# Kernel tuning notes

Measured on AMD Instinct MI355X. Metric: run time of the kernel, lower is better.

The kernel has to match this reference:

```python
import jax, jax.numpy as jnp
import numpy as np

TOPK = 5
LAMBDA_ALIGN_K = 16.0
MOM = 0.9          # EMA momentum
DEFAULT_SCORE = 0.5  # EMA bank default (bank starts empty)
EPS = 1e-8
NEG = 1.0e9


def pairwise_cosine(X):
    # torch F.normalize: X / max(||X||, eps)
    n = jnp.linalg.norm(X, axis=-1, keepdims=True)
    Xn = X / jnp.maximum(n, EPS)
    sim = Xn @ Xn.T
    return jnp.clip(sim, -1.0 + EPS, 1.0 - EPS)


def knn_mask(sim, allowed_base, topk=TOPK):
    B = sim.shape[0]
    eye = jnp.eye(B, dtype=sim.dtype)
    allowed = allowed_base * (1.0 - eye)
    masked = sim - NEG * eye
    masked = jnp.where(allowed < 0.5, -NEG, masked)
    masked = jnp.where(masked < 0.0, -NEG, masked)
    cand = (masked > 0).sum(axis=1)
    k = min(topk, max(B - 1, 1))
    keep_row = (cand >= topk).astype(sim.dtype)
    keep = keep_row[:, None] * keep_row[None, :]
    idx = jax.lax.top_k(masked, k)[1]                       # [B, k]
    M = jnp.zeros_like(sim).at[jnp.arange(B)[:, None], idx].set(1.0)
    M = jnp.maximum(M, M.T)
    return M * allowed * keep


def build_intra(sim, same, topk=TOPK):
    M = knn_mask(sim, same, topk)
    A = jnp.maximum(sim * M, 0.0) * same
    return A, M


def pga_loss(feats_sub, labels_sub):
    # feats_sub: [L, b, d]
    L = feats_sub.shape[0]
    same = (labels_sub[:, None] == labels_sub[None, :]).astype(jnp.float32)
    sims = jax.vmap(pairwise_cosine)(feats_sub)             # [L, b, b]
    A, M = jax.vmap(lambda s: build_intra(s, same))(sims)   # [L, b, b] each

    # EMA degree-based scores (no-grad in original; bank starts empty so
    # fetch-after-update == mom*default + (1-mom)*score_cur)
    S_intra = jnp.maximum(sims * same, 0.0)
    deg = jnp.maximum((S_intra > 0).sum(axis=2).astype(jnp.float32), 1.0)
    score_cur = jax.nn.sigmoid(S_intra.sum(axis=2) / deg)   # [L, b]
    ema = jax.lax.stop_gradient(MOM * DEFAULT_SCORE + (1.0 - MOM) * score_cur)

    # layer-pair masked MSE alignment, target detached
    A_deep = A[1:]
    A_tgt = jax.lax.stop_gradient(A[:-1])
    M_eff = jnp.maximum(M[:-1], M[1:])                      # [L-1, b, b]
    W = ema[:-1, :, None] * ema[:-1, None, :]               # [L-1, b, b]
    diff2 = (A_deep - A_tgt) ** 2 * W
    num = (diff2 * M_eff).sum(axis=(1, 2))
    den = jnp.maximum((M_eff * W).sum(axis=(1, 2)), EPS)
    terms = jnp.where(M_eff.sum(axis=(1, 2)) > 0, num / den, 0.0)
    raw = terms.sum() / max(L - 1, 1)
    return LAMBDA_ALIGN_K * raw


def setup_inputs() -> dict:
    key = jax.random.key(0)
    k1, k2 = jax.random.split(key)
    feats_final = jax.random.normal(k1, (8, 2048, 512), dtype=jnp.float32)
    labels = jax.random.randint(k2, (2048,), 0, 128).astype(jnp.int64)
    sample_ids = jnp.arange(2048, dtype=jnp.int64)
    return {"feats_final": feats_final, "labels": labels, "sample_ids": sample_ids}


def reference(feats_final, labels, sample_ids):
    # candidate subset from last layer (no-grad in original)
    X_last = feats_final[-1]
    S_last = pairwise_cosine(X_last)
    same_full = (labels[:, None] == labels[None, :]).astype(jnp.float32)
    _, M_last = build_intra(S_last, same_full)
    cand_mask = (M_last > 0).sum(axis=1) > 0
    idx_sub = jnp.nonzero(cand_mask)[0]  # eager (concrete) subselection
    feats_sub = feats_final[:, idx_sub]  # [L, b, d]
    labels_sub = labels[idx_sub]
    return pga_loss(feats_sub, labels_sub)
```

## Files before the change

### kernel.cpp

```cpp
#include <hip/hip_runtime.h>
#include <cmath>

#define NB   2048
#define ND   512
#define NL   8
#define NLAB 128
#define MAXM 64
#define TOPK_ 5
#define NTH  256
#define MAXSLOT 9
#define GSTRIDE (MAXM*MAXM)

__global__ __launch_bounds__(NTH) void k_bucket(
    const int* __restrict__ labels, int* __restrict__ members,
    int* __restrict__ cnt)
{
    __shared__ int cnts[NTH];
    int c = blockIdx.x, tid = threadIdx.x;
    int my[8]; int n = 0;
    int base_i = tid * 8;
    for (int t = 0; t < 8; ++t) {
        int i = base_i + t;
        if (labels[i] == c) my[n++] = i;
    }
    cnts[tid] = n;
    __syncthreads();
    for (int off = 1; off < NTH; off <<= 1) {
        int v = (tid >= off) ? cnts[tid - off] : 0;
        __syncthreads();
        cnts[tid] += v;
        __syncthreads();
    }
    int excl = cnts[tid] - n;
    if (tid == 0) cnt[c] = cnts[NTH - 1];
    for (int t = 0; t < n; ++t) {
        int slot = excl + t;
        if (slot < MAXM) members[c * MAXM + slot] = my[t];
    }
}

__global__ __launch_bounds__(NTH) void k_gram(
    const float* __restrict__ feats, const int* __restrict__ members,
    const int* __restrict__ cnt, float* __restrict__ G)
{
    __shared__ float Xt[MAXM][132];
    __shared__ int g_s[MAXM];
    int c = blockIdx.x, l = blockIdx.y, tid = threadIdx.x;
    int m = cnt[c]; if (m > MAXM) m = MAXM;
    if (m == 0) return;
    if (tid < m) g_s[tid] = members[c * MAXM + tid];
    __syncthreads();
    const float* X = feats + (size_t)l * NB * ND;

    const int P = m * (m + 1) / 2;
    float acc0[MAXSLOT], acc1[MAXSLOT];
    short is_[MAXSLOT], js_[MAXSLOT];
    int ns = 0;
    for (int p = tid; p < P; p += NTH) {
        int i = (int)((sqrtf(8.0f * (float)p + 1.0f) - 1.0f) * 0.5f);
        while (((i + 1) * (i + 2)) / 2 <= p) ++i;
        while ((i * (i + 1)) / 2 > p) --i;
        is_[ns] = (short)i;
        js_[ns] = (short)(p - (i * (i + 1)) / 2);
        acc0[ns] = 0.0f; acc1[ns] = 0.0f;
        ++ns;
    }
    for (int kc = 0; kc < ND; kc += 128) {
        if (kc) __syncthreads();
        for (int idx = tid; idx < (m << 5); idx += NTH) {
            int i = idx >> 5, k4 = idx & 31;
            float4 v = *(const float4*)(X + ((size_t)g_s[i] << 9) + kc + (k4 << 2));
            *(float4*)&Xt[i][k4 << 2] = v;
        }
        __syncthreads();
        for (int s = 0; s < ns; ++s) {
            int i = is_[s], j = js_[s];
            float a0 = acc0[s], a1 = acc1[s];
            #pragma unroll
            for (int k4 = 0; k4 < 32; ++k4) {
                float4 a = *(const float4*)&Xt[i][k4 << 2];
                float4 b = *(const float4*)&Xt[j][k4 << 2];
                a0 = fmaf(a.x, b.x, a0); a1 = fmaf(a.y, b.y, a1);
                a0 = fmaf(a.z, b.z, a0); a1 = fmaf(a.w, b.w, a1);
            }
            acc0[s] = a0; acc1[s] = a1;
        }
    }
    float* Gc = G + ((size_t)l * NLAB + c) * GSTRIDE;
    for (int s = 0; s < ns; ++s) {
        int i = is_[s], j = js_[s];
        float v = acc0[s] + acc1[s];
        Gc[i * MAXM + j] = v;
        Gc[j * MAXM + i] = v;
    }
}

__global__ __launch_bounds__(NTH) void k_phase1(
    const float* __restrict__ G, const int* __restrict__ cnt,
    unsigned long long* __restrict__ insub)
{
    __shared__ float Gs[64][65];
    __shared__ float rinv[64];
    __shared__ unsigned long long tops_s[64];
    __shared__ unsigned char keep_s[64];
    int c = blockIdx.x, tid = threadIdx.x;
    int m = cnt[c]; if (m > MAXM) m = MAXM;
    if (m == 0) { if (tid == 0) insub[c] = 0ull; return; }
    const float* Gc = G + ((size_t)7 * NLAB + c) * GSTRIDE;
    if (tid < m) rinv[tid] = 1.0f / fmaxf(sqrtf(Gc[tid * MAXM + tid]), 1e-8f);
    __syncthreads();
    for (int idx = tid; idx < (m << 6); idx += NTH) {
        int i = idx >> 6, j = idx & 63;
        if (j < m) {
            float v = Gc[idx] * rinv[i] * rinv[j];
            Gs[i][j] = fminf(fmaxf(v, -1.0f), 1.0f);
        }
    }
    __syncthreads();

    unsigned long long tops = 0ull; bool keep = false;
    if (tid < m) {
        int cand = 0;
        for (int j = 0; j < m; ++j)
            if (j != tid && Gs[tid][j] > 0.0f) ++cand;
        keep = (cand >= TOPK_);
        if (keep) {
            for (int r = 0; r < TOPK_; ++r) {
                float bv = 0.0f; int bj = -1;
                for (int j = 0; j < m; ++j) {
                    if (j == tid || ((tops >> j) & 1ull)) continue;
                    float v = Gs[tid][j];
                    if (v > 0.0f && v > bv) { bv = v; bj = j; }
                }
                if (bj >= 0) tops |= (1ull << bj);
            }
        }
        keep_s[tid] = keep ? 1 : 0; tops_s[tid] = tops;
    }
    __syncthreads();
    unsigned long long Mrow = 0ull;
    if (tid < m && keep) {
        for (int j = 0; j < m; ++j) {
            if (j == tid || !keep_s[j]) continue;
            if (((tops >> j) & 1ull) || ((tops_s[j] >> tid) & 1ull)) Mrow |= (1ull << j);
        }
    }
    if (tid < 64) {
        unsigned long long b = __ballot(Mrow != 0ull);
        if (tid == 0) insub[c] = b;
    }
}

__global__ __launch_bounds__(NTH) void k_decide(
    const float* __restrict__ G, const int* __restrict__ cnt,
    const unsigned long long* __restrict__ insub,
    unsigned long long* __restrict__ Mbits, float* __restrict__ ema)
{
    __shared__ float Gs[64][65];
    __shared__ float rinv[64];
    __shared__ unsigned long long tops_s[64];
    __shared__ unsigned char keep_s[64];
    int c = blockIdx.x, l = blockIdx.y, tid = threadIdx.x;
    int m = cnt[c]; if (m > MAXM) m = MAXM;
    if (m == 0) return;
    unsigned long long sub = insub[c];
    const float* Gc = G + ((size_t)l * NLAB + c) * GSTRIDE;
    if (tid < m) rinv[tid] = 1.0f / fmaxf(sqrtf(Gc[tid * MAXM + tid]), 1e-8f);
    __syncthreads();
    for (int idx = tid; idx < (m << 6); idx += NTH) {
        int i = idx >> 6, j = idx & 63;
        if (j < m) {
            float v = Gc[idx] * rinv[i] * rinv[j];
            Gs[i][j] = fminf(fmaxf(v, -1.0f), 1.0f);
        }
    }
    __syncthreads();

    unsigned long long tops = 0ull; bool keep = false; bool act = false;
    if (tid < m) {
        act = (sub >> tid) & 1ull;
        int cand = 0;
        if (act) {
            for (int j = 0; j < m; ++j)
                if (j != tid && ((sub >> j) & 1ull) && Gs[tid][j] > 0.0f) ++cand;
        }
        keep = act && (cand >= TOPK_);
        if (keep) {
            for (int r = 0; r < TOPK_; ++r) {
                float bv = 0.0f; int bj = -1;
                for (int j = 0; j < m; ++j) {
                    if (j == tid || !((sub >> j) & 1ull) || ((tops >> j) & 1ull)) continue;
                    float v = Gs[tid][j];
                    if (v > 0.0f && v > bv) { bv = v; bj = j; }
                }
                if (bj >= 0) tops |= (1ull << bj);
            }
        }
        keep_s[tid] = keep ? 1 : 0; tops_s[tid] = tops;
    }
    __syncthreads();
    if (tid < m) {
        unsigned long long Mrow = 0ull;
        if (keep) {
            for (int j = 0; j < m; ++j) {
                if (j == tid || !keep_s[j]) continue;
                if (((tops >> j) & 1ull) || ((tops_s[j] >> tid) & 1ull)) Mrow |= (1ull << j);
            }
        }
        Mbits[((size_t)l * NLAB + c) * MAXM + tid] = Mrow;
        float emaval = 0.0f;
        if (act) {
            float rs = 0.0f; int dg = 0;
            for (int j = 0; j < m; ++j) {
                if ((sub >> j) & 1ull) {
                    float v = Gs[tid][j];
                    if (v > 0.0f) { rs += v; ++dg; }
                }
            }
            float deg = (float)(dg > 0 ? dg : 1);
            float score = 1.0f / (1.0f + expf(-rs / deg));
            emaval = 0.45f + 0.1f * score;
        }
        ema[((size_t)l * NLAB + c) * MAXM + tid] = emaval;
    }
}

__global__ __launch_bounds__(NTH) void k_pairs(
    const float* __restrict__ G, const int* __restrict__ cnt,
    const unsigned long long* __restrict__ Mbits, const float* __restrict__ ema,
    float* __restrict__ partial)
{
    __shared__ float r0[64], r1[64];
    __shared__ unsigned long long M0s[64], M1s[64];
    __shared__ float es[64];
    __shared__ float red[12];
    int c = blockIdx.x, p = blockIdx.y, tid = threadIdx.x;
    int m = cnt[c]; if (m > MAXM) m = MAXM;
    const float* G0 = G + ((size_t)p       * NLAB + c) * GSTRIDE;
    const float* G1 = G + ((size_t)(p + 1) * NLAB + c) * GSTRIDE;
    if (tid < m) {
        M0s[tid] = Mbits[((size_t)p * NLAB + c) * MAXM + tid];
        M1s[tid] = Mbits[((size_t)(p + 1) * NLAB + c) * MAXM + tid];
        es[tid]  = ema[((size_t)p * NLAB + c) * MAXM + tid];
        r0[tid]  = 1.0f / fmaxf(sqrtf(G0[tid * MAXM + tid]), 1e-8f);
        r1[tid]  = 1.0f / fmaxf(sqrtf(G1[tid * MAXM + tid]), 1e-8f);
    }
    __syncthreads();
    float fn = 0.0f, fd = 0.0f, fc = 0.0f;
    for (int idx = tid; idx < (m << 6); idx += NTH) {
        int i = idx >> 6, j = idx & 63;
        if (j >= m) continue;
        bool b0 = (M0s[i] >> j) & 1ull;
        bool b1 = (M1s[i] >> j) & 1ull;
        if (b0 | b1) {
            float v0 = b0 ? fminf(fmaxf(G0[idx] * r0[i] * r0[j], -1.0f), 1.0f) : 0.0f;
            float v1 = b1 ? fminf(fmaxf(G1[idx] * r1[i] * r1[j], -1.0f), 1.0f) : 0.0f;
            float w = es[i] * es[j];
            float d = v1 - v0;
            fn = fmaf(d * d, w, fn);
            fd += w;
            fc += 1.0f;
        }
    }
    for (int off = 32; off > 0; off >>= 1) {
        fn += __shfl_down(fn, off);
        fd += __shfl_down(fd, off);
        fc += __shfl_down(fc, off);
    }
    int w = tid >> 6;
    if ((tid & 63) == 0) { red[w * 3] = fn; red[w * 3 + 1] = fd; red[w * 3 + 2] = fc; }
    __syncthreads();
    if (tid == 0) {
        float* dst = partial + ((size_t)p * NLAB + c) * 4;
        dst[0] = red[0] + red[3] + red[6] + red[9];
        dst[1] = red[1] + red[4] + red[7] + red[10];
        dst[2] = red[2] + red[5] + red[8] + red[11];
    }
}

__global__ void k_final(const float* __restrict__ partial, float* __restrict__ out)
{
    int tid = threadIdx.x;
    float total = 0.0f;
    for (int p = 0; p < NL - 1; ++p) {
        float n = 0.0f, d = 0.0f, cc = 0.0f;
        for (int c = tid; c < NLAB; c += 64) {
            const float* src = partial + ((size_t)p * NLAB + c) * 4;
            n += src[0]; d += src[1]; cc += src[2];
        }
        for (int off = 32; off > 0; off >>= 1) {
            n += __shfl_down(n, off);
            d += __shfl_down(d, off);
            cc += __shfl_down(cc, off);
        }
        if (tid == 0 && cc > 0.0f) total += n / fmaxf(d, 1e-8f);
    }
    if (tid == 0) out[0] = 16.0f * total / 7.0f;
}

extern "C" void kernel_launch(void* const* d_in, const int* in_sizes, int n_in,
                              void* d_out, int out_size, void* d_ws, size_t ws_size,
                              hipStream_t stream) {
    const float* feats  = (const float*)d_in[0];
    const int*   labels = (const int*)d_in[1];
    char* w = (char*)d_ws;
    int* members              = (int*)(w);
    int* cnt                  = (int*)(w + 32768);
    unsigned long long* insub = (unsigned long long*)(w + 33280);
    unsigned long long* Mbits = (unsigned long long*)(w + 34304);
    float* ema                = (float*)(w + 558592);
    float* G                  = (float*)(w + 821248);
    float* partial            = (float*)(w + 821248 + (size_t)NL * NLAB * GSTRIDE * 4);
    float* out                = (float*)d_out;

    k_bucket<<<NLAB, NTH, 0, stream>>>(labels, members, cnt);
    k_gram  <<<dim3(NLAB, NL), NTH, 0, stream>>>(feats, members, cnt, G);
    k_phase1<<<NLAB, NTH, 0, stream>>>(G, cnt, insub);
    k_decide<<<dim3(NLAB, NL), NTH, 0, stream>>>(G, cnt, insub, Mbits, ema);
    k_pairs <<<dim3(NLAB, NL - 1), NTH, 0, stream>>>(G, cnt, Mbits, ema, partial);
    k_final <<<1, 64, 0, stream>>>(partial, out);
}
```

Measured before the change: 147.0 us.

## Fuse six kernels into two: bucket into gram, post-gram stages into one per-label kernel

Label bucketing is folded into the Gram kernel, so each block scans labels itself instead of reading a separate members array. Phase1, per-layer decide, pair alignment and the final reduction are merged into one kernel with a block per label, which keeps masks and EMA values in shared memory. A ticket atomic lets the last finishing block do the global reduction. This removes four launches and the global round trips for intermediates, but the per-label work now runs on only 128 blocks in sequence over layers instead of 1024 parallel blocks.

```diff
diff --git a/kernel.cpp b/kernel.cpp
--- a/kernel.cpp
+++ b/kernel.cpp
@@ -11,14 +11,17 @@
 #define MAXSLOT 9
 #define GSTRIDE (MAXM*MAXM)
 
-__global__ __launch_bounds__(NTH) void k_bucket(
-    const int* __restrict__ labels, int* __restrict__ members,
-    int* __restrict__ cnt)
+__global__ __launch_bounds__(NTH) void k_gram(
+    const float* __restrict__ feats, const int* __restrict__ labels,
+    float* __restrict__ G, unsigned* __restrict__ ticket)
 {
     __shared__ int cnts[NTH];
-    int c = blockIdx.x, tid = threadIdx.x;
-    int my[8]; int n = 0;
-    int base_i = tid * 8;
+    __shared__ int g_s[MAXM];
+    __shared__ float Xt[MAXM][132];
+    int c = blockIdx.x, l = blockIdx.y, tid = threadIdx.x;
+    if (c == 0 && l == 0 && tid == 0) *ticket = 0u;
+
+    int my[8]; int n = 0; int base_i = tid * 8;
     for (int t = 0; t < 8; ++t) {
         int i = base_i + t;
         if (labels[i] == c) my[n++] = i;
@@ -32,26 +35,15 @@
         __syncthreads();
     }
     int excl = cnts[tid] - n;
-    if (tid == 0) cnt[c] = cnts[NTH - 1];
+    int m = cnts[NTH - 1]; if (m > MAXM) m = MAXM;
     for (int t = 0; t < n; ++t) {
         int slot = excl + t;
-        if (slot < MAXM) members[c * MAXM + slot] = my[t];
-    }
-}
-
-__global__ __launch_bounds__(NTH) void k_gram(
-    const float* __restrict__ feats, const int* __restrict__ members,
-    const int* __restrict__ cnt, float* __restrict__ G)
-{
-    __shared__ float Xt[MAXM][132];
-    __shared__ int g_s[MAXM];
-    int c = blockIdx.x, l = blockIdx.y, tid = threadIdx.x;
-    int m = cnt[c]; if (m > MAXM) m = MAXM;
+        if (slot < MAXM) g_s[slot] = my[t];
+    }
+    __syncthreads();
     if (m == 0) return;
-    if (tid < m) g_s[tid] = members[c * MAXM + tid];
-    __syncthreads();
+
     const float* X = feats + (size_t)l * NB * ND;
-
     const int P = m * (m + 1) / 2;
     float acc0[MAXSLOT], acc1[MAXSLOT];
     short is_[MAXSLOT], js_[MAXSLOT];
@@ -95,207 +87,210 @@
     }
 }
 
-__global__ __launch_bounds__(NTH) void k_phase1(
-    const float* __restrict__ G, const int* __restrict__ cnt,
-    unsigned long long* __restrict__ insub)
+__global__ __launch_bounds__(NTH) void k_rest(
+    const float* __restrict__ G, const int* __restrict__ labels,
+    float* __restrict__ partial,
+    unsigned* __restrict__ ticket, float* __restrict__ out)
 {
     __shared__ float Gs[64][65];
-    __shared__ float rinv[64];
+    __shared__ float rinv8[NL][64];
+    __shared__ unsigned long long Mb[NL][64];
+    __shared__ float es8[NL][64];
     __shared__ unsigned long long tops_s[64];
     __shared__ unsigned char keep_s[64];
+    __shared__ int cnts[NTH];
+    __shared__ unsigned long long insub_sh;
+    __shared__ float red[12];
+    __shared__ unsigned done_s;
     int c = blockIdx.x, tid = threadIdx.x;
-    int m = cnt[c]; if (m > MAXM) m = MAXM;
-    if (m == 0) { if (tid == 0) insub[c] = 0ull; return; }
-    const float* Gc = G + ((size_t)7 * NLAB + c) * GSTRIDE;
-    if (tid < m) rinv[tid] = 1.0f / fmaxf(sqrtf(Gc[tid * MAXM + tid]), 1e-8f);
-    __syncthreads();
-    for (int idx = tid; idx < (m << 6); idx += NTH) {
-        int i = idx >> 6, j = idx & 63;
-        if (j < m) {
-            float v = Gc[idx] * rinv[i] * rinv[j];
-            Gs[i][j] = fminf(fmaxf(v, -1.0f), 1.0f);
-        }
-    }
-    __syncthreads();
-
-    unsigned long long tops = 0ull; bool keep = false;
-    if (tid < m) {
-        int cand = 0;
-        for (int j = 0; j < m; ++j)
-            if (j != tid && Gs[tid][j] > 0.0f) ++cand;
-        keep = (cand >= TOPK_);
-        if (keep) {
-            for (int r = 0; r < TOPK_; ++r) {
-                float bv = 0.0f; int bj = -1;
+
+    int n = 0; int base_i = tid * 8;
+    for (int t = 0; t < 8; ++t) if (labels[base_i + t] == c) ++n;
+    cnts[tid] = n;
+    __syncthreads();
+    for (int off = NTH / 2; off > 0; off >>= 1) {
+        if (tid < off) cnts[tid] += cnts[tid + off];
+        __syncthreads();
+    }
+    int m = cnts[0]; if (m > MAXM) m = MAXM;
+
+    if (m > 0) {
+        const float* Gc7 = G + ((size_t)7 * NLAB + c) * GSTRIDE;
+        if (tid < m) rinv8[7][tid] = 1.0f / fmaxf(sqrtf(Gc7[tid * MAXM + tid]), 1e-8f);
+        __syncthreads();
+        for (int idx = tid; idx < (m << 6); idx += NTH) {
+            int i = idx >> 6, j = idx & 63;
+            if (j < m) {
+                float v = Gc7[idx] * rinv8[7][i] * rinv8[7][j];
+                Gs[i][j] = fminf(fmaxf(v, -1.0f), 1.0f);
+            }
+        }
+        __syncthreads();
+        {
+            unsigned long long tops = 0ull; bool keep = false;
+            if (tid < m) {
+                int cand = 0;
+                for (int j = 0; j < m; ++j)
+                    if (j != tid && Gs[tid][j] > 0.0f) ++cand;
+                keep = (cand >= TOPK_);
+                if (keep) {
+                    for (int r = 0; r < TOPK_; ++r) {
+                        float bv = 0.0f; int bj = -1;
+                        for (int j = 0; j < m; ++j) {
+                            if (j == tid || ((tops >> j) & 1ull)) continue;
+                            float v = Gs[tid][j];
+                            if (v > 0.0f && v > bv) { bv = v; bj = j; }
+                        }
+                        if (bj >= 0) tops |= (1ull << bj);
+                    }
+                }
+                keep_s[tid] = keep ? 1 : 0; tops_s[tid] = tops;
+            }
+            __syncthreads();
+            unsigned long long Mrow = 0ull;
+            if (tid < m && keep) {
                 for (int j = 0; j < m; ++j) {
-                    if (j == tid || ((tops >> j) & 1ull)) continue;
-                    float v = Gs[tid][j];
-                    if (v > 0.0f && v > bv) { bv = v; bj = j; }
-                }
-                if (bj >= 0) tops |= (1ull << bj);
-            }
-        }
-        keep_s[tid] = keep ? 1 : 0; tops_s[tid] = tops;
-    }
-    __syncthreads();
-    unsigned long long Mrow = 0ull;
-    if (tid < m && keep) {
-        for (int j = 0; j < m; ++j) {
-            if (j == tid || !keep_s[j]) continue;
-            if (((tops >> j) & 1ull) || ((tops_s[j] >> tid) & 1ull)) Mrow |= (1ull << j);
-        }
-    }
-    if (tid < 64) {
-        unsigned long long b = __ballot(Mrow != 0ull);
-        if (tid == 0) insub[c] = b;
-    }
-}
-
-__global__ __launch_bounds__(NTH) void k_decide(
-    const float* __restrict__ G, const int* __restrict__ cnt,
-    const unsigned long long* __restrict__ insub,
-    unsigned long long* __restrict__ Mbits, float* __restrict__ ema)
-{
-    __shared__ float Gs[64][65];
-    __shared__ float rinv[64];
-    __shared__ unsigned long long tops_s[64];
-    __shared__ unsigned char keep_s[64];
-    int c = blockIdx.x, l = blockIdx.y, tid = threadIdx.x;
-    int m = cnt[c]; if (m > MAXM) m = MAXM;
-    if (m == 0) return;
-    unsigned long long sub = insub[c];
-    const float* Gc = G + ((size_t)l * NLAB + c) * GSTRIDE;
-    if (tid < m) rinv[tid] = 1.0f / fmaxf(sqrtf(Gc[tid * MAXM + tid]), 1e-8f);
-    __syncthreads();
-    for (int idx = tid; idx < (m << 6); idx += NTH) {
-        int i = idx >> 6, j = idx & 63;
-        if (j < m) {
-            float v = Gc[idx] * rinv[i] * rinv[j];
-            Gs[i][j] = fminf(fmaxf(v, -1.0f), 1.0f);
-        }
-    }
-    __syncthreads();
-
-    unsigned long long tops = 0ull; bool keep = false; bool act = false;
-    if (tid < m) {
-        act = (sub >> tid) & 1ull;
-        int cand = 0;
-        if (act) {
-            for (int j = 0; j < m; ++j)
-                if (j != tid && ((sub >> j) & 1ull) && Gs[tid][j] > 0.0f) ++cand;
-        }
-        keep = act && (cand >= TOPK_);
-        if (keep) {
-            for (int r = 0; r < TOPK_; ++r) {
-                float bv = 0.0f; int bj = -1;
-                for (int j = 0; j < m; ++j) {
-                    if (j == tid || !((sub >> j) & 1ull) || ((tops >> j) & 1ull)) continue;
-                    float v = Gs[tid][j];
-                    if (v > 0.0f && v > bv) { bv = v; bj = j; }
-                }
-                if (bj >= 0) tops |= (1ull << bj);
-            }
-        }
-        keep_s[tid] = keep ? 1 : 0; tops_s[tid] = tops;
-    }
-    __syncthreads();
-    if (tid < m) {
-        unsigned long long Mrow = 0ull;
-        if (keep) {
-            for (int j = 0; j < m; ++j) {
-                if (j == tid || !keep_s[j]) continue;
-                if (((tops >> j) & 1ull) || ((tops_s[j] >> tid) & 1ull)) Mrow |= (1ull << j);
-            }
-        }
-        Mbits[((size_t)l * NLAB + c) * MAXM + tid] = Mrow;
-        float emaval = 0.0f;
-        if (act) {
-            float rs = 0.0f; int dg = 0;
-            for (int j = 0; j < m; ++j) {
-                if ((sub >> j) & 1ull) {
-                    float v = Gs[tid][j];
-                    if (v > 0.0f) { rs += v; ++dg; }
-                }
-            }
-            float deg = (float)(dg > 0 ? dg : 1);
-            float score = 1.0f / (1.0f + expf(-rs / deg));
-            emaval = 0.45f + 0.1f * score;
-        }
-        ema[((size_t)l * NLAB + c) * MAXM + tid] = emaval;
-    }
-}
-
-__global__ __launch_bounds__(NTH) void k_pairs(
-    const float* __restrict__ G, const int* __restrict__ cnt,
-    const unsigned long long* __restrict__ Mbits, const float* __restrict__ ema,
-    float* __restrict__ partial)
-{
-    __shared__ float r0[64], r1[64];
-    __shared__ unsigned long long M0s[64], M1s[64];
-    __shared__ float es[64];
-    __shared__ float red[12];
-    int c = blockIdx.x, p = blockIdx.y, tid = threadIdx.x;
-    int m = cnt[c]; if (m > MAXM) m = MAXM;
-    const float* G0 = G + ((size_t)p       * NLAB + c) * GSTRIDE;
-    const float* G1 = G + ((size_t)(p + 1) * NLAB + c) * GSTRIDE;
-    if (tid < m) {
-        M0s[tid] = Mbits[((size_t)p * NLAB + c) * MAXM + tid];
-        M1s[tid] = Mbits[((size_t)(p + 1) * NLAB + c) * MAXM + tid];
-        es[tid]  = ema[((size_t)p * NLAB + c) * MAXM + tid];
-        r0[tid]  = 1.0f / fmaxf(sqrtf(G0[tid * MAXM + tid]), 1e-8f);
-        r1[tid]  = 1.0f / fmaxf(sqrtf(G1[tid * MAXM + tid]), 1e-8f);
-    }
-    __syncthreads();
-    float fn = 0.0f, fd = 0.0f, fc = 0.0f;
-    for (int idx = tid; idx < (m << 6); idx += NTH) {
-        int i = idx >> 6, j = idx & 63;
-        if (j >= m) continue;
-        bool b0 = (M0s[i] >> j) & 1ull;
-        bool b1 = (M1s[i] >> j) & 1ull;
-        if (b0 | b1) {
-            float v0 = b0 ? fminf(fmaxf(G0[idx] * r0[i] * r0[j], -1.0f), 1.0f) : 0.0f;
-            float v1 = b1 ? fminf(fmaxf(G1[idx] * r1[i] * r1[j], -1.0f), 1.0f) : 0.0f;
-            float w = es[i] * es[j];
-            float d = v1 - v0;
-            fn = fmaf(d * d, w, fn);
-            fd += w;
-            fc += 1.0f;
-        }
-    }
-    for (int off = 32; off > 0; off >>= 1) {
-        fn += __shfl_down(fn, off);
-        fd += __shfl_down(fd, off);
-        fc += __shfl_down(fc, off);
-    }
-    int w = tid >> 6;
-    if ((tid & 63) == 0) { red[w * 3] = fn; red[w * 3 + 1] = fd; red[w * 3 + 2] = fc; }
-    __syncthreads();
-    if (tid == 0) {
-        float* dst = partial + ((size_t)p * NLAB + c) * 4;
-        dst[0] = red[0] + red[3] + red[6] + red[9];
-        dst[1] = red[1] + red[4] + red[7] + red[10];
-        dst[2] = red[2] + red[5] + red[8] + red[11];
-    }
-}
-
-__global__ void k_final(const float* __restrict__ partial, float* __restrict__ out)
-{
-    int tid = threadIdx.x;
-    float total = 0.0f;
-    for (int p = 0; p < NL - 1; ++p) {
-        float n = 0.0f, d = 0.0f, cc = 0.0f;
-        for (int c = tid; c < NLAB; c += 64) {
-            const float* src = partial + ((size_t)p * NLAB + c) * 4;
-            n += src[0]; d += src[1]; cc += src[2];
-        }
-        for (int off = 32; off > 0; off >>= 1) {
-            n += __shfl_down(n, off);
-            d += __shfl_down(d, off);
-            cc += __shfl_down(cc, off);
-        }
-        if (tid == 0 && cc > 0.0f) total += n / fmaxf(d, 1e-8f);
-    }
-    if (tid == 0) out[0] = 16.0f * total / 7.0f;
+                    if (j == tid || !keep_s[j]) continue;
+                    if (((tops >> j) & 1ull) || ((tops_s[j] >> tid) & 1ull)) Mrow |= (1ull << j);
+                }
+            }
+            if (tid < 64) {
+                unsigned long long b = __ballot(Mrow != 0ull);
+                if (tid == 0) insub_sh = b;
+            }
+            __syncthreads();
+        }
+        unsigned long long sub = insub_sh;
+
+        for (int l = 0; l < NL; ++l) {
+            const float* Gc = G + ((size_t)l * NLAB + c) * GSTRIDE;
+            if (tid < m) rinv8[l][tid] = 1.0f / fmaxf(sqrtf(Gc[tid * MAXM + tid]), 1e-8f);
+            __syncthreads();
+            for (int idx = tid; idx < (m << 6); idx += NTH) {
+                int i = idx >> 6, j = idx & 63;
+                if (j < m) {
+                    float v = Gc[idx] * rinv8[l][i] * rinv8[l][j];
+                    Gs[i][j] = fminf(fmaxf(v, -1.0f), 1.0f);
+                }
+            }
+            __syncthreads();
+            unsigned long long tops = 0ull; bool keep = false; bool act = false;
+            if (tid < m) {
+                act = (sub >> tid) & 1ull;
+                int cand = 0;
+                if (act) {
+                    for (int j = 0; j < m; ++j)
+                        if (j != tid && ((sub >> j) & 1ull) && Gs[tid][j] > 0.0f) ++cand;
+                }
+                keep = act && (cand >= TOPK_);
+                if (keep) {
+                    for (int r = 0; r < TOPK_; ++r) {
+                        float bv = 0.0f; int bj = -1;
+                        for (int j = 0; j < m; ++j) {
+                            if (j == tid || !((sub >> j) & 1ull) || ((tops >> j) & 1ull)) continue;
+                            float v = Gs[tid][j];
+                            if (v > 0.0f && v > bv) { bv = v; bj = j; }
+                        }
+                        if (bj >= 0) tops |= (1ull << bj);
+                    }
+                }
+                keep_s[tid] = keep ? 1 : 0; tops_s[tid] = tops;
+            }
+            __syncthreads();
+            if (tid < m) {
+                unsigned long long Mrow = 0ull;
+                if (keep) {
+                    for (int j = 0; j < m; ++j) {
+                        if (j == tid || !keep_s[j]) continue;
+                        if (((tops >> j) & 1ull) || ((tops_s[j] >> tid) & 1ull)) Mrow |= (1ull << j);
+                    }
+                }
+                Mb[l][tid] = Mrow;
+                float emaval = 0.0f;
+                if (act) {
+                    float rs = 0.0f; int dg = 0;
+                    for (int j = 0; j < m; ++j) {
+                        if ((sub >> j) & 1ull) {
+                            float v = Gs[tid][j];
+                            if (v > 0.0f) { rs += v; ++dg; }
+                        }
+                    }
+                    float deg = (float)(dg > 0 ? dg : 1);
+                    float score = 1.0f / (1.0f + expf(-rs / deg));
+                    emaval = 0.45f + 0.1f * score;
+                }
+                es8[l][tid] = emaval;
+            }
+            __syncthreads();
+        }
+
+        for (int p = 0; p < NL - 1; ++p) {
+            const float* G0 = G + ((size_t)p       * NLAB + c) * GSTRIDE;
+            const float* G1 = G + ((size_t)(p + 1) * NLAB + c) * GSTRIDE;
+            float fn = 0.0f, fd = 0.0f, fc = 0.0f;
+            for (int idx = tid; idx < (m << 6); idx += NTH) {
+                int i = idx >> 6, j = idx & 63;
+                if (j >= m) continue;
+                bool b0 = (Mb[p][i] >> j) & 1ull;
+                bool b1 = (Mb[p + 1][i] >> j) & 1ull;
+                if (b0 | b1) {
+                    float v0 = b0 ? fminf(fmaxf(G0[idx] * rinv8[p][i] * rinv8[p][j], -1.0f), 1.0f) : 0.0f;
+                    float v1 = b1 ? fminf(fmaxf(G1[idx] * rinv8[p + 1][i] * rinv8[p + 1][j], -1.0f), 1.0f) : 0.0f;
+                    float w = es8[p][i] * es8[p][j];
+                    float d = v1 - v0;
+                    fn = fmaf(d * d, w, fn);
+                    fd += w;
+                    fc += 1.0f;
+                }
+            }
+            for (int off = 32; off > 0; off >>= 1) {
+                fn += __shfl_down(fn, off);
+                fd += __shfl_down(fd, off);
+                fc += __shfl_down(fc, off);
+            }
+            int w = tid >> 6;
+            if ((tid & 63) == 0) { red[w * 3] = fn; red[w * 3 + 1] = fd; red[w * 3 + 2] = fc; }
+            __syncthreads();
+            if (tid == 0) {
+                float* dst = partial + ((size_t)p * NLAB + c) * 4;
+                dst[0] = red[0] + red[3] + red[6] + red[9];
+                dst[1] = red[1] + red[4] + red[7] + red[10];
+                dst[2] = red[2] + red[5] + red[8] + red[11];
+            }
+            __syncthreads();
+        }
+    } else {
+        if (tid < NL - 1) {
+            float* dst = partial + ((size_t)tid * NLAB + c) * 4;
+            dst[0] = 0.0f; dst[1] = 0.0f; dst[2] = 0.0f;
+        }
+        __syncthreads();
+    }
+
+    __threadfence();
+    __syncthreads();
+    if (tid == 0) done_s = atomicAdd(ticket, 1u);
+    __syncthreads();
+    if (done_s == NLAB - 1) {
+        __threadfence();
+        if (tid < 64) {
+            float total = 0.0f;
+            for (int p = 0; p < NL - 1; ++p) {
+                float nn = 0.0f, dd = 0.0f, cc = 0.0f;
+                for (int cc_i = tid; cc_i < NLAB; cc_i += 64) {
+                    const float* src = partial + ((size_t)p * NLAB + cc_i) * 4;
+                    nn += src[0]; dd += src[1]; cc += src[2];
+                }
+                for (int off = 32; off > 0; off >>= 1) {
+                    nn += __shfl_down(nn, off);
+                    dd += __shfl_down(dd, off);
+                    cc += __shfl_down(cc, off);
+                }
+                if (tid == 0 && cc > 0.0f) total += nn / fmaxf(dd, 1e-8f);
+            }
+            if (tid == 0) out[0] = 16.0f * total / 7.0f;
+        }
+    }
 }
 
 extern "C" void kernel_launch(void* const* d_in, const int* in_sizes, int n_in,
@@ -304,19 +299,11 @@
     const float* feats  = (const float*)d_in[0];
     const int*   labels = (const int*)d_in[1];
     char* w = (char*)d_ws;
-    int* members              = (int*)(w);
-    int* cnt                  = (int*)(w + 32768);
-    unsigned long long* insub = (unsigned long long*)(w + 33280);
-    unsigned long long* Mbits = (unsigned long long*)(w + 34304);
-    float* ema                = (float*)(w + 558592);
-    float* G                  = (float*)(w + 821248);
-    float* partial            = (float*)(w + 821248 + (size_t)NL * NLAB * GSTRIDE * 4);
-    float* out                = (float*)d_out;
-
-    k_bucket<<<NLAB, NTH, 0, stream>>>(labels, members, cnt);
-    k_gram  <<<dim3(NLAB, NL), NTH, 0, stream>>>(feats, members, cnt, G);
-    k_phase1<<<NLAB, NTH, 0, stream>>>(G, cnt, insub);
-    k_decide<<<dim3(NLAB, NL), NTH, 0, stream>>>(G, cnt, insub, Mbits, ema);
-    k_pairs <<<dim3(NLAB, NL - 1), NTH, 0, stream>>>(G, cnt, Mbits, ema, partial);
-    k_final <<<1, 64, 0, stream>>>(partial, out);
+    float*    G       = (float*)(w);
+    float*    partial = (float*)(w + (size_t)NL * NLAB * GSTRIDE * 4);
+    unsigned* ticket  = (unsigned*)(w + (size_t)NL * NLAB * GSTRIDE * 4 + 14336);
+    float*    out     = (float*)d_out;
+
+    k_gram<<<dim3(NLAB, NL), NTH, 0, stream>>>(feats, labels, G, ticket);
+    k_rest<<<NLAB, NTH, 0, stream>>>(G, labels, partial, ticket, out);
 }
```

After: 303.1 us. 2.06x slower.
